# Kernel tuning notes

Hardware: AMD Instinct MI355X
Metric: run time of the kernel (lower is better)

The kernel has to match this reference:

```python
import jax, jax.numpy as jnp
import numpy as np

M = 128  # template / canvas size (hardcoded in the module)


def _pair_indices(nodes_per_image):
    # Static (host-side) ragged pair construction, mirroring the Python loop
    # in the torch forward. Returns compressed index arrays for valid pairs.
    npi = np.asarray(nodes_per_image)
    idx_a, idx_b, batch, valid = [], [], [], []
    off = 0
    for b, n in enumerate(npi.tolist()):
        a = np.repeat(np.arange(n), n) + off   # repeat_interleave
        c = np.tile(np.arange(n), n) + off     # .repeat(n, 1)
        idx_a.append(a); idx_b.append(c)
        batch.append(np.full(n * n, b))
        if n > 1:
            v = np.triu(np.ones((n, n)), 1).astype(bool).reshape(-1)
        else:
            v = np.zeros((n * n,), bool)
        valid.append(v)
        off += n
    return (np.concatenate(idx_a), np.concatenate(idx_b),
            np.concatenate(batch), np.concatenate(valid))


def _grid_sample_bilinear(img, gx, gy):
    # img [O, M, M]; gx, gy [O, H, W] in [-1, 1]; align_corners=True, zero padding
    ix = (gx + 1.0) * 0.5 * (M - 1)
    iy = (gy + 1.0) * 0.5 * (M - 1)
    x0 = jnp.floor(ix); y0 = jnp.floor(iy)
    wx = ix - x0; wy = iy - y0
    out = jnp.zeros_like(gx)
    corners = ((0, 0, (1 - wy) * (1 - wx)), (0, 1, (1 - wy) * wx),
               (1, 0, wy * (1 - wx)), (1, 1, wy * wx))
    for dy, dx, w in corners:
        xi = x0 + dx; yi = y0 + dy
        inb = (xi >= 0) & (xi <= M - 1) & (yi >= 0) & (yi <= M - 1)
        xc = jnp.clip(xi, 0, M - 1).astype(jnp.int32)
        yc = jnp.clip(yi, 0, M - 1).astype(jnp.int32)
        v = jax.vmap(lambda m, yy, xx: m[yy, xx])(img, yc, xc)
        out = out + w * jnp.where(inb, v, 0.0)
    return out


def masks_to_layout(vecs, boxes, masks, obj_to_img, num_images, H):
    # sg2im-style: warp each mask into its box, scale by vec, scatter-add per image
    x0 = boxes[:, 0][:, None, None]; y0 = boxes[:, 1][:, None, None]
    x1 = boxes[:, 2][:, None, None]; y1 = boxes[:, 3][:, None, None]
    X = jnp.linspace(0.0, 1.0, H)[None, None, :]   # [1,1,W]
    Y = jnp.linspace(0.0, 1.0, H)[None, :, None]   # [1,H,1]
    gx = ((X - x0) / (x1 - x0)) * 2.0 - 1.0        # [O,1,W]
    gy = ((Y - y0) / (y1 - y0)) * 2.0 - 1.0        # [O,H,1]
    O = boxes.shape[0]
    gx = jnp.broadcast_to(gx, (O, H, H))
    gy = jnp.broadcast_to(gy, (O, H, H))
    sampled = _grid_sample_bilinear(masks, gx, gy)           # [O,H,W]
    sampled = sampled * vecs[:, 0][:, None, None]            # D = 1 channel
    out = jax.ops.segment_sum(sampled, obj_to_img, num_segments=num_images)
    return out[:, None]  # [B,1,H,W] (segment_sum already zero-pads empty images)


def _forward(nodes, adj_mat, nodes_per_image):
    ii = jnp.arange(M)
    # eye(128) max-pooled with k=11, s=1, p=5 -> band of half-width 10
    line_template = (jnp.abs(ii[:, None] - ii[None, :]) <= 10).astype(jnp.float32)
    idx_a, idx_b, batch_ids, valid = _pair_indices(nodes_per_image)
    sel = np.nonzero(valid)[0]
    idx_a = idx_a[sel]; idx_b = idx_b[sel]
    obj_to_img = jnp.asarray(batch_ids[sel], dtype=jnp.int32)
    boxes = jnp.concatenate([nodes[idx_a], nodes[idx_b]], axis=1)  # [O,4]
    vecs = adj_mat[sel]                                            # [O,1]
    B = int(np.asarray(nodes_per_image).shape[0])
    dual_slope = (jnp.abs((boxes[:, 3] - boxes[:, 1]) / (jnp.abs(boxes[:, 2] - boxes[:, 0]) + 1e-6))
                  + jnp.abs((boxes[:, 2] - boxes[:, 0]) / (jnp.abs(boxes[:, 3] - boxes[:, 1]) + 1e-6)))
    t = jnp.clip(2.0 * jax.nn.sigmoid(0.03 * (dual_slope - 2.0)) - 1.0, 0.0, 1.0)
    t = t[:, None, None]
    masks = (1.0 - t) * line_template[None, :, :] + t  # rect_template == ones
    img = masks_to_layout(vecs, boxes, masks, obj_to_img, B, M)
    return jnp.clip(img, 0.0, 1.0)


def setup_inputs() -> dict:
    key = jax.random.key(0)
    k1, k2 = jax.random.split(key)
    B, n = 24, 16
    nodes = jax.random.uniform(k1, (B * n, 2), dtype=jnp.float32)       # [384,2] in [0,1]
    adj_mat = jax.random.uniform(k2, (B * n * n, 1), dtype=jnp.float32)  # [6144,1]
    nodes_per_image = np.full((B,), n, dtype=np.int64)  # static ragged sizes
    return {"nodes": nodes, "adj_mat": adj_mat, "nodes_per_image": nodes_per_image}


def reference(nodes, adj_mat, nodes_per_image):
    return _forward(nodes, adj_mat, nodes_per_image)
```

## Files before the change

### kernel.cpp

```cpp
#include <hip/hip_runtime.h>

#define MM     128
#define NN     16
#define NPAIR  120
#define NIMG   24
#define BPI    32
#define NLIST  8
#define CAP    121

__global__ __launch_bounds__(512, 6) void g2i_kernel(
    const float* __restrict__ nodes,
    const float* __restrict__ adj,
    float* __restrict__ out)
{
    __shared__ float4 s_AB[NLIST][CAP * 2];
    __shared__ float  s_c [NLIST][CAP];
    __shared__ int    s_cnt[NLIST];

    const int img  = blockIdx.x >> 5;
    const int bp   = blockIdx.x & 31;
    const int tid  = threadIdx.x;
    const int lane = tid & 63;

    if (tid < NLIST) s_cnt[tid] = 0;
    __syncthreads();

    if (tid < NPAIR) {
        const int k = tid;
        int i = (int)(15.5f - sqrtf(240.25f - 2.0f * (float)k));
        int oi = (i * (31 - i)) >> 1;
        if (k < oi) { --i; oi = (i * (31 - i)) >> 1; }
        else { const int oi1 = ((i + 1) * (30 - i)) >> 1; if (k >= oi1) { ++i; oi = oi1; } }
        const int j = i + 1 + (k - oi);

        const float2 na = ((const float2*)nodes)[img * NN + i];
        const float2 nb = ((const float2*)nodes)[img * NN + j];
        const float x0 = na.x, y0 = na.y, x1 = nb.x, y1 = nb.y;
        const float dx = x1 - x0, dy = y1 - y0;

        const float ya  = 127.0f * y0 - dy;
        const float yb  = ya + 129.0f * dy;
        const float ylo = fminf(ya, yb) - 0.5f;
        const float yhi = fmaxf(ya, yb) + 0.5f;

        const float rA0 = (float)(2 * bp);
        const float rB0 = (float)(2 * (bp + 32));
        const bool anyy = ((yhi >= rA0 && ylo <= rA0 + 1.0f) ||
                           (yhi >= rB0 && ylo <= rB0 + 1.0f));

        if (anyy) {
            const float adx = fabsf(dx), ady = fabsf(dy);
            const float ds  = ady * __builtin_amdgcn_rcpf(adx + 1e-6f)
                            + adx * __builtin_amdgcn_rcpf(ady + 1e-6f);
            const float e = __expf(-0.03f * (ds - 2.0f));
            float t = fmaf(2.0f, __builtin_amdgcn_rcpf(1.0f + e), -1.0f);
            t = fminf(fmaxf(t, 0.0f), 1.0f);
            const float vec = adj[img * NN * NN + i * NN + j];
            const float p = vec * t, q = vec * (1.0f - t);

            const float cax = __builtin_amdgcn_rcpf(dx);
            const float cbx = -127.0f * x0 * cax;
            const float cay = __builtin_amdgcn_rcpf(dy);
            const float cby = -127.0f * y0 * cay;

            const float xa  = 127.0f * x0 - dx;
            const float xb  = xa + 129.0f * dx;
            const float xlo = fminf(xa, xb) - 0.5f;
            const float xhi = fmaxf(xa, xb) + 0.5f;
            bool whit[2];
            whit[0] = (xhi >= -0.5f) && (xlo <=  63.5f);
            whit[1] = (xhi >= 63.5f) && (xlo <= 127.5f);
            const float wb0 = cbx;
            const float wb1 = fmaf(64.0f, cax, cbx);

            #pragma unroll
            for (int st = 0; st < 2; ++st) {
                const float row0 = st ? rB0 : rA0;
                #pragma unroll
                for (int r = 0; r < 2; ++r) {
                    const float ry = row0 + (float)r;
                    const bool hy = (yhi >= ry) && (ylo <= ry);

                    const float iy  = fmaf(ry, cay, cby);
                    const float y0f = floorf(iy);
                    const float wy  = iy - y0f;
                    const float ey0 = (y0f >=  0.0f && y0f <= 127.0f) ? (1.0f - wy) : 0.0f;
                    const float ey1 = (y0f >= -1.0f && y0f <= 126.0f) ? wy          : 0.0f;
                    const float A0 = fmaxf(0.0f,   y0f - 10.0f);
                    const float B0 = fminf(127.0f, y0f + 10.0f);
                    const float A1 = fmaxf(0.0f,   y0f -  9.0f);
                    const float B1 = fminf(127.0f, y0f + 11.0f);
                    const float pe  = p * (ey0 + ey1);
                    const float qe0 = q * ey0, qe1 = q * ey1;

                    #pragma unroll
                    for (int w = 0; w < 2; ++w) {
                        const bool hit = hy && whit[w];
                        const unsigned long long m = __ballot(hit);
                        if (m) {
                            const int lid = st * 4 + w * 2 + r;
                            const int leader = __ffsll(m) - 1;
                            int base = 0;
                            if (lane == leader) base = atomicAdd(&s_cnt[lid], (int)__popcll(m));
                            base = __shfl(base, leader);
                            if (hit) {
                                const int slot = base + (int)__popcll(m & ((1ull << lane) - 1ull));
                                const float wb = w ? wb1 : wb0;
                                s_AB[lid][slot * 2 + 0] =
                                    make_float4(wb + 1.0f - A0, B0 - A0 + 2.0f,
                                                wb + 1.0f - A1, B1 - A1 + 2.0f);
                                s_AB[lid][slot * 2 + 1] = make_float4(pe, qe0, qe1, A0);
                                s_c [lid][slot] = cax;
                            }
                        }
                    }
                }
            }
        }
    }
    __syncthreads();

    const int wv = tid >> 6;
    const int st = wv >> 2;
    const int w  = (wv >> 1) & 1;
    const int r  = wv & 1;
    const int py = (st ? (bp + 32) : bp) * 2 + r;
    const int px = w * 64 + lane;
    const float fl = (float)lane;
    const int cnt = s_cnt[wv];

    const float4* __restrict__ AB = &s_AB[wv][0];
    const float*  __restrict__ C  = &s_c[wv][0];

    float acc = 0.0f;
    float4 a_n = AB[0], b_n = AB[1];
    float  c_n = C[0];

    for (int s = 0; s < cnt; ++s) {
        const float4 a = a_n, b = b_n;
        const float ca = c_n;
        a_n = AB[(s + 1) * 2 + 0];
        b_n = AB[(s + 1) * 2 + 1];
        c_n = C[s + 1];

        const float z0 = fmaf(fl, ca, a.x);
        const float s0 = a.y - z0;
        const float z1 = fmaf(fl, ca, a.z);
        const float s1 = a.w - z1;
        const float zs = z0 + b.w;
        const float t0 = __builtin_amdgcn_fmed3f(fminf(z0, s0), 0.0f, 1.0f);
        const float t1 = __builtin_amdgcn_fmed3f(fminf(z1, s1), 0.0f, 1.0f);
        const float ts = __builtin_amdgcn_fmed3f(fminf(zs, 129.0f - zs), 0.0f, 1.0f);
        acc = fmaf(b.x, ts, acc);
        acc = fmaf(b.y, t0, acc);
        acc = fmaf(b.z, t1, acc);
    }

    acc = fminf(fmaxf(acc, 0.0f), 1.0f);
    out[(size_t)img * (MM * MM) + py * MM + px] = acc;
}

extern "C" void kernel_launch(void* const* d_in, const int* in_sizes, int n_in,
                              void* d_out, int out_size, void* d_ws, size_t ws_size,
                              hipStream_t stream) {
    const float* nodes = (const float*)d_in[0];
    const float* adj   = (const float*)d_in[1];
    float* out = (float*)d_out;
    g2i_kernel<<<dim3(NIMG * BPI), dim3(512), 0, stream>>>(nodes, adj, out);
}
```

Measured before the change: 64.91 us.

## Compact per-segment LDS records to float4 plus packed half2 weights

Each list entry shrinks from two float4 plus a float to one float4 (slope, offset, y0f, pe) and one packed half2 of the q weights. The inner loop recomputes the clamp ranges from ix and y0f using abs-distance forms. Entries whose vertical weights sum to zero are now skipped. The aim is less LDS traffic and shared memory per block, traded for a few extra ALU ops per entry, half-precision rounding of the q weights, and a possible tolerance risk.

```diff
diff --git a/kernel.cpp b/kernel.cpp
--- a/kernel.cpp
+++ b/kernel.cpp
@@ -1,4 +1,5 @@
 #include <hip/hip_runtime.h>
+#include <hip/hip_fp16.h>
 
 #define MM     128
 #define NN     16
@@ -13,9 +14,9 @@
     const float* __restrict__ adj,
     float* __restrict__ out)
 {
-    __shared__ float4 s_AB[NLIST][CAP * 2];
-    __shared__ float  s_c [NLIST][CAP];
-    __shared__ int    s_cnt[NLIST];
+    __shared__ float4   s_A[NLIST][CAP];
+    __shared__ unsigned s_B[NLIST][CAP];
+    __shared__ int      s_cnt[NLIST];
 
     const int img  = blockIdx.x >> 5;
     const int bp   = blockIdx.x & 31;
@@ -70,8 +71,9 @@
             bool whit[2];
             whit[0] = (xhi >= -0.5f) && (xlo <=  63.5f);
             whit[1] = (xhi >= 63.5f) && (xlo <= 127.5f);
-            const float wb0 = cbx;
-            const float wb1 = fmaf(64.0f, cax, cbx);
+            float wb[2];
+            wb[0] = cbx;
+            wb[1] = fmaf(64.0f, cax, cbx);
 
             #pragma unroll
             for (int st = 0; st < 2; ++st) {
@@ -79,23 +81,21 @@
                 #pragma unroll
                 for (int r = 0; r < 2; ++r) {
                     const float ry = row0 + (float)r;
-                    const bool hy = (yhi >= ry) && (ylo <= ry);
-
                     const float iy  = fmaf(ry, cay, cby);
                     const float y0f = floorf(iy);
                     const float wy  = iy - y0f;
                     const float ey0 = (y0f >=  0.0f && y0f <= 127.0f) ? (1.0f - wy) : 0.0f;
                     const float ey1 = (y0f >= -1.0f && y0f <= 126.0f) ? wy          : 0.0f;
-                    const float A0 = fmaxf(0.0f,   y0f - 10.0f);
-                    const float B0 = fminf(127.0f, y0f + 10.0f);
-                    const float A1 = fmaxf(0.0f,   y0f -  9.0f);
-                    const float B1 = fminf(127.0f, y0f + 11.0f);
-                    const float pe  = p * (ey0 + ey1);
-                    const float qe0 = q * ey0, qe1 = q * ey1;
+                    const float eys = ey0 + ey1;
+                    const float pe  = p * eys;
+                    const bool  emit = (yhi >= ry) && (ylo <= ry) && (eys > 0.0f);
+
+                    union { __half2 h; unsigned u; } qp;
+                    qp.h = __halves2half2(__float2half(q * ey0), __float2half(q * ey1));
 
                     #pragma unroll
                     for (int w = 0; w < 2; ++w) {
-                        const bool hit = hy && whit[w];
+                        const bool hit = emit && whit[w];
                         const unsigned long long m = __ballot(hit);
                         if (m) {
                             const int lid = st * 4 + w * 2 + r;
@@ -105,12 +105,8 @@
                             base = __shfl(base, leader);
                             if (hit) {
                                 const int slot = base + (int)__popcll(m & ((1ull << lane) - 1ull));
-                                const float wb = w ? wb1 : wb0;
-                                s_AB[lid][slot * 2 + 0] =
-                                    make_float4(wb + 1.0f - A0, B0 - A0 + 2.0f,
-                                                wb + 1.0f - A1, B1 - A1 + 2.0f);
-                                s_AB[lid][slot * 2 + 1] = make_float4(pe, qe0, qe1, A0);
-                                s_c [lid][slot] = cax;
+                                s_A[lid][slot] = make_float4(cax, wb[w], y0f, pe);
+                                s_B[lid][slot] = qp.u;
                             }
                         }
                     }
@@ -129,31 +125,34 @@
     const float fl = (float)lane;
     const int cnt = s_cnt[wv];
 
-    const float4* __restrict__ AB = &s_AB[wv][0];
-    const float*  __restrict__ C  = &s_c[wv][0];
+    const float4*   __restrict__ A = &s_A[wv][0];
+    const unsigned* __restrict__ B = &s_B[wv][0];
 
     float acc = 0.0f;
-    float4 a_n = AB[0], b_n = AB[1];
-    float  c_n = C[0];
+    float4   a_n = A[0];
+    unsigned q_n = B[0];
 
     for (int s = 0; s < cnt; ++s) {
-        const float4 a = a_n, b = b_n;
-        const float ca = c_n;
-        a_n = AB[(s + 1) * 2 + 0];
-        b_n = AB[(s + 1) * 2 + 1];
-        c_n = C[s + 1];
+        const float4   a = a_n;
+        const unsigned qu = q_n;
+        a_n = A[s + 1];
+        q_n = B[s + 1];
 
-        const float z0 = fmaf(fl, ca, a.x);
-        const float s0 = a.y - z0;
-        const float z1 = fmaf(fl, ca, a.z);
-        const float s1 = a.w - z1;
-        const float zs = z0 + b.w;
-        const float t0 = __builtin_amdgcn_fmed3f(fminf(z0, s0), 0.0f, 1.0f);
-        const float t1 = __builtin_amdgcn_fmed3f(fminf(z1, s1), 0.0f, 1.0f);
-        const float ts = __builtin_amdgcn_fmed3f(fminf(zs, 129.0f - zs), 0.0f, 1.0f);
-        acc = fmaf(b.x, ts, acc);
-        acc = fmaf(b.y, t0, acc);
-        acc = fmaf(b.z, t1, acc);
+        const float ix = fmaf(fl, a.x, a.y);
+        const float F  = fminf(ix + 1.0f, 128.0f - ix);
+        const float h  = ix - a.z;
+        const float a0 = 11.0f - fabsf(h);
+        const float a1 = 11.0f - fabsf(h - 1.0f);
+        const float ts = __builtin_amdgcn_fmed3f(F, 0.0f, 1.0f);
+        const float t0 = __builtin_amdgcn_fmed3f(fminf(a0, F), 0.0f, 1.0f);
+        const float t1 = __builtin_amdgcn_fmed3f(fminf(a1, F), 0.0f, 1.0f);
+
+        union { unsigned u; __half2 h2; } qp; qp.u = qu;
+        const float2 qf = __half22float2(qp.h2);
+
+        acc = fmaf(a.w, ts, acc);
+        acc = fmaf(qf.x, t0, acc);
+        acc = fmaf(qf.y, t1, acc);
     }
 
     acc = fminf(fmaxf(acc, 0.0f), 1.0f);
```

Measured after the change: 65.19 us, median of 2. Within noise of the previous version (+0.4%).
